# Kernel optimization log

Measured on AMD Instinct MI355X. Metric: run time of the kernel, lower is better.

Reference implementation:

```python
import jax, jax.numpy as jnp
import numpy as np

N_NODES = 100000


def _gcn_layer(h, W, b, src, dst, norm, n):
    # h: [N, Fin] -> [N, Fout]; normalized scatter-add aggregation (GCNConv)
    hw = h @ W
    msg = norm[:, None] * hw[src]
    out = jax.ops.segment_sum(msg, dst, num_segments=n)
    return out + b


def setup_inputs() -> dict:
    key = jax.random.key(0)
    k = jax.random.split(key, 10)
    N, E, P, F = N_NODES, 3200000, 500000, 128
    x = jax.random.normal(k[0], (N, F), dtype=jnp.float32)
    edge_index = jax.random.randint(k[1], (2, E), 0, N, dtype=jnp.int64)
    pred_edges = jax.random.randint(k[2], (P, 2), 0, N, dtype=jnp.int64)
    # Glorot-ish init for learned params
    W1 = jax.random.normal(k[3], (F, 16), dtype=jnp.float32) / np.sqrt(F)
    b1 = jnp.zeros((16,), dtype=jnp.float32)
    W2 = jax.random.normal(k[4], (16, 8), dtype=jnp.float32) / np.sqrt(16.0)
    b2 = jnp.zeros((8,), dtype=jnp.float32)
    Wl = jax.random.normal(k[5], (8, 1), dtype=jnp.float32) / np.sqrt(8.0)
    bl = jnp.zeros((1,), dtype=jnp.float32)
    return {"x": x, "edge_index": edge_index, "pred_edges": pred_edges,
            "W1": W1, "b1": b1, "W2": W2, "b2": b2, "Wl": Wl, "bl": bl}


def reference(x, edge_index, pred_edges, W1, b1, W2, b2, Wl, bl):
    n = x.shape[0]
    # GCN norm with self-loops: A_hat = D^{-1/2}(A+I)D^{-1/2}
    loop = jnp.arange(n, dtype=edge_index.dtype)
    src = jnp.concatenate([edge_index[0], loop])
    dst = jnp.concatenate([edge_index[1], loop])
    deg = jax.ops.segment_sum(jnp.ones_like(dst, dtype=x.dtype), dst, num_segments=n)
    dinv = jnp.where(deg > 0, jax.lax.rsqrt(deg), 0.0)
    norm = dinv[src] * dinv[dst]

    h = _gcn_layer(x, W1, b1, src, dst, norm, n)   # [N, 16]
    h = _gcn_layer(h, W2, b2, src, dst, norm, n)   # [N, 8]
    z = jax.nn.sigmoid(h @ Wl + bl)                # [N, 1]
    m = z[pred_edges]                              # [P, 2, 1]
    pred = m[:, 0, 0] * m[:, 1, 0]                 # [P]
    return pred
```

## Files before the change

kernel.cpp:

```cpp
#include <hip/hip_runtime.h>
#include <hip/hip_fp16.h>
#include <math.h>

#define BSHIFT 8
#define BUCK   256
#define TILE   8192
#define CAP    12288

typedef _Float16 f16x2 __attribute__((ext_vector_type(2)));
typedef _Float16 f16x4 __attribute__((ext_vector_type(4)));
typedef _Float16 f16x8 __attribute__((ext_vector_type(8)));
typedef float    f32x4 __attribute__((ext_vector_type(4)));


__global__ __launch_bounds__(256) void k_curinit(int* __restrict__ bcursor, int nbuk) {
    int b = blockIdx.x * 256 + threadIdx.x;
    if (b < nbuk) bcursor[b] = b * CAP;
}

__global__ __launch_bounds__(1024) void k_binscatter(const int* __restrict__ src,
                                                     const int* __restrict__ dst,
                                                     int* __restrict__ bcursor,
                                                     int* __restrict__ binned, int E, int nbuk) {
    __shared__ int            payload[TILE];
    __shared__ unsigned short bid16[TILE];
    __shared__ int cnt[512];
    __shared__ int lstart[512];
    __shared__ int gbase[512];
    __shared__ int wsum[8];
    int t = threadIdx.x;
    int tile0 = blockIdx.x * TILE;
    int tileE = min(TILE, E - tile0);
    if (t < 512) cnt[t] = 0;
    __syncthreads();
    int d[8], s[8];
    int base = t * 8;
    if (base + 8 <= tileE) {
        const int4* d4 = (const int4*)(dst + tile0 + base);
        const int4* s4 = (const int4*)(src + tile0 + base);
        int4 da = d4[0], db = d4[1];
        int4 sa = s4[0], sb = s4[1];
        d[0] = da.x; d[1] = da.y; d[2] = da.z; d[3] = da.w;
        d[4] = db.x; d[5] = db.y; d[6] = db.z; d[7] = db.w;
        s[0] = sa.x; s[1] = sa.y; s[2] = sa.z; s[3] = sa.w;
        s[4] = sb.x; s[5] = sb.y; s[6] = sb.z; s[7] = sb.w;
    } else {
#pragma unroll
        for (int q = 0; q < 8; ++q) {
            int idx = base + q;
            if (idx < tileE) { d[q] = dst[tile0 + idx]; s[q] = src[tile0 + idx]; }
            else d[q] = -1;
        }
    }
#pragma unroll
    for (int q = 0; q < 8; ++q)
        if (d[q] >= 0) atomicAdd(&cnt[d[q] >> BSHIFT], 1);
    __syncthreads();
    int c = 0, ex = 0;
    if (t < 512) {
        c = cnt[t];
        int v = c;
#pragma unroll
        for (int off = 1; off < 64; off <<= 1) {
            int u = __shfl_up(v, off, 64);
            if ((t & 63) >= off) v += u;
        }
        if ((t & 63) == 63) wsum[t >> 6] = v;
        ex = v - c;
    }
    __syncthreads();
    if (t == 0) {
        int run = 0;
#pragma unroll
        for (int w = 0; w < 8; ++w) { int u = wsum[w]; wsum[w] = run; run += u; }
    }
    __syncthreads();
    if (t < 512) {
        ex += wsum[t >> 6];
        gbase[t] = c ? atomicAdd(&bcursor[t], c) : 0;
        lstart[t] = ex;
        cnt[t] = ex;
    }
    __syncthreads();
#pragma unroll
    for (int q = 0; q < 8; ++q) {
        if (d[q] >= 0) {
            int b = d[q] >> BSHIFT;
            int lp = atomicAdd(&cnt[b], 1);
            payload[lp] = ((d[q] & (BUCK - 1)) << 17) | s[q];
            bid16[lp] = (unsigned short)b;
        }
    }
    __syncthreads();
    for (int k = t; k < tileE; k += 1024) {
        int b = bid16[k];
        int ga = gbase[b] + (k - lstart[b]);
        if (ga < (b + 1) * CAP)
            binned[ga] = payload[k];
    }
}

__global__ __launch_bounds__(1024) void k_sortbucket(const int* __restrict__ bcursor,
                                                     const int* __restrict__ binned,
                                                     int* __restrict__ csr_src,
                                                     int* __restrict__ rowstart,
                                                     int* __restrict__ rowend,
                                                     float* __restrict__ dinv, int N) {
    __shared__ int cnt[BUCK];
    __shared__ int cur[BUCK];
    __shared__ int wsum[4];
    int b = blockIdx.x, t = threadIdx.x;
    if (t < BUCK) cnt[t] = 0;
    __syncthreads();
    int beg = b * CAP;
    int end = min(bcursor[b], beg + CAP);
    int v[12];
#pragma unroll
    for (int q = 0; q < 12; ++q) {
        int e = beg + q * 1024 + t;
        v[q] = (e < end) ? binned[e] : -1;
    }
#pragma unroll
    for (int q = 0; q < 12; ++q)
        if (v[q] >= 0) atomicAdd(&cnt[v[q] >> 17], 1);
    __syncthreads();
    int c = 0, ex = 0;
    if (t < BUCK) {
        c = cnt[t];
        int s = c;
#pragma unroll
        for (int off = 1; off < 64; off <<= 1) {
            int u = __shfl_up(s, off, 64);
            if ((t & 63) >= off) s += u;
        }
        if ((t & 63) == 63) wsum[t >> 6] = s;
        ex = s - c;
    }
    __syncthreads();
    if (t == 0) {
        int run = 0;
#pragma unroll
        for (int w = 0; w < 4; ++w) { int u = wsum[w]; wsum[w] = run; run += u; }
    }
    __syncthreads();
    if (t < BUCK) {
        ex += wsum[t >> 6];
        cur[t] = ex;
        int node = b * BUCK + t;
        if (node < N) {
            rowstart[node] = beg + ex;
            rowend[node]   = beg + ex + c;
            dinv[node] = rsqrtf((float)(c + 1));
        }
    }
    __syncthreads();
#pragma unroll
    for (int q = 0; q < 12; ++q) {
        if (v[q] >= 0) {
            int pos = atomicAdd(&cur[v[q] >> 17], 1);
            csr_src[beg + pos] = v[q] & 0x1FFFF;
        }
    }
}


__global__ __launch_bounds__(256) void k_gemm1(const float* __restrict__ x,
                                               const float* __restrict__ W1,
                                               const float* __restrict__ dinv,
                                               __half* __restrict__ hw1h, int N) {
    __shared__ _Float16 sX[64 * 136];
    __shared__ _Float16 sW[16 * 136];
    __shared__ float    sDi[64];
    __shared__ _Float16 sOut[64 * 16];
    int t = threadIdx.x;
    int row0 = blockIdx.x * 64;
    for (int e = t; e < 2048; e += 256) {
        int n = e & 15, k = e >> 4;
        sW[n * 136 + k] = (_Float16)W1[k * 16 + n];
    }
    const float4* x4 = (const float4*)x;
#pragma unroll
    for (int q = 0; q < 8; ++q) {
        int e = q * 256 + t;
        int r = e >> 5, c4 = e & 31;
        int gr = row0 + r;
        float4 v = (gr < N) ? x4[(size_t)gr * 32 + c4] : make_float4(0.f, 0.f, 0.f, 0.f);
        f16x4 hv = {(_Float16)v.x, (_Float16)v.y, (_Float16)v.z, (_Float16)v.w};
        *(f16x4*)&sX[r * 136 + c4 * 4] = hv;
    }
    if (t < 64) sDi[t] = (row0 + t < N) ? dinv[row0 + t] : 0.f;
    __syncthreads();
    int w = t >> 6, l = t & 63;
    int m = l & 15, quad = l >> 4;
    f32x4 acc = {0.f, 0.f, 0.f, 0.f};
#pragma unroll
    for (int kc = 0; kc < 4; ++kc) {
        f16x8 a = *(const f16x8*)&sX[(w * 16 + m) * 136 + kc * 32 + quad * 8];
        f16x8 b = *(const f16x8*)&sW[m * 136 + kc * 32 + quad * 8];
        acc = __builtin_amdgcn_mfma_f32_16x16x32_f16(a, b, acc, 0, 0, 0);
    }
#pragma unroll
    for (int r = 0; r < 4; ++r) {
        int nl = w * 16 + quad * 4 + r;
        sOut[nl * 16 + m] = (_Float16)(acc[r] * sDi[nl]);
    }
    __syncthreads();
    int nn = t >> 2, ch = t & 3;
    int gn = row0 + nn;
    if (gn < N)
        *(float2*)&hw1h[(size_t)gn * 16 + ch * 4] = *(float2*)&sOut[nn * 16 + ch * 4];
}

__global__ __launch_bounds__(256) void k_agg1c(const int* __restrict__ rowstart,
                                               const int* __restrict__ rowend,
                                               const int* __restrict__ csr_src,
                                               const f16x8* __restrict__ hw1v,
                                               const float* __restrict__ W2,
                                               const float* __restrict__ b1,
                                               __half* __restrict__ hw2h, int N) {
    __shared__ float sW[128], sb[16];
    int t = threadIdx.x;
    if (t < 128) sW[t] = W2[t];
    if (t < 16)  sb[t] = b1[t];
    __syncthreads();
    int q = t >> 2, j = t & 3;
    int i = blockIdx.x * 64 + q;
    if (i >= N) return;
    int beg = rowstart[i], end = rowend[i];
    float di = rsqrtf((float)(end - beg + 1));
    float a[16];
#pragma unroll
    for (int d = 0; d < 16; ++d) a[d] = 0.f;
    int c0 = beg;
    for (; c0 + 16 <= end; c0 += 16) {
        int s4[4];
#pragma unroll
        for (int m = 0; m < 4; ++m) s4[m] = csr_src[c0 + 4 * j + m];
        f16x8 lo[4], hi[4];
#pragma unroll
        for (int m = 0; m < 4; ++m) {
            lo[m] = hw1v[2 * (size_t)s4[m]];
            hi[m] = hw1v[2 * (size_t)s4[m] + 1];
        }
#pragma unroll
        for (int m = 0; m < 4; ++m) {
#pragma unroll
            for (int d = 0; d < 8; ++d) {
                a[d]     += (float)lo[m][d];
                a[8 + d] += (float)hi[m][d];
            }
        }
    }
    for (int c = c0 + j; c < end; c += 4) {
        int s = csr_src[c];
        f16x8 lo = hw1v[2 * (size_t)s];
        f16x8 hi = hw1v[2 * (size_t)s + 1];
#pragma unroll
        for (int d = 0; d < 8; ++d) {
            a[d]     += (float)lo[d];
            a[8 + d] += (float)hi[d];
        }
    }
    if (j == 0) {
        f16x8 lo = hw1v[2 * (size_t)i];
        f16x8 hi = hw1v[2 * (size_t)i + 1];
#pragma unroll
        for (int d = 0; d < 8; ++d) {
            a[d]     += (float)lo[d];
            a[8 + d] += (float)hi[d];
        }
    }
#pragma unroll
    for (int d = 0; d < 16; ++d) a[d] += __shfl_xor(a[d], 1, 4);
#pragma unroll
    for (int d = 0; d < 16; ++d) a[d] += __shfl_xor(a[d], 2, 4);
    float o0 = 0.f, o1 = 0.f;
#pragma unroll
    for (int k = 0; k < 16; ++k) {
        float hv = di * a[k] + sb[k];
        o0 += hv * sW[k * 8 + 2 * j];
        o1 += hv * sW[k * 8 + 2 * j + 1];
    }
    f16x2 ho = {(_Float16)(di * o0), (_Float16)(di * o1)};
    *(f16x2*)&hw2h[(size_t)i * 8 + 2 * j] = ho;
}

__global__ __launch_bounds__(256) void k_agg2c(const int* __restrict__ rowstart,
                                               const int* __restrict__ rowend,
                                               const int* __restrict__ csr_src,
                                               const f16x8* __restrict__ hw2v,
                                               const float* __restrict__ Wl,
                                               const float* __restrict__ b2,
                                               const float* __restrict__ bl,
                                               float* __restrict__ z, int N) {
    __shared__ float sW[8], sb[8], sbl;
    int t = threadIdx.x;
    if (t < 8) { sW[t] = Wl[t]; sb[t] = b2[t]; }
    if (t == 0) sbl = bl[0];
    __syncthreads();
    int q = t >> 2, j = t & 3;
    int i = blockIdx.x * 64 + q;
    if (i >= N) return;
    int beg = rowstart[i], end = rowend[i];
    float di = rsqrtf((float)(end - beg + 1));
    float a[8];
#pragma unroll
    for (int d = 0; d < 8; ++d) a[d] = 0.f;
    int c0 = beg;
    for (; c0 + 16 <= end; c0 += 16) {
        int s4[4];
#pragma unroll
        for (int m = 0; m < 4; ++m) s4[m] = csr_src[c0 + 4 * j + m];
        f16x8 gv[4];
#pragma unroll
        for (int m = 0; m < 4; ++m) gv[m] = hw2v[(size_t)s4[m]];
#pragma unroll
        for (int m = 0; m < 4; ++m)
#pragma unroll
            for (int d = 0; d < 8; ++d) a[d] += (float)gv[m][d];
    }
    for (int c = c0 + j; c < end; c += 4) {
        f16x8 gv = hw2v[(size_t)csr_src[c]];
#pragma unroll
        for (int d = 0; d < 8; ++d) a[d] += (float)gv[d];
    }
    if (j == 0) {
        f16x8 self = hw2v[(size_t)i];
#pragma unroll
        for (int d = 0; d < 8; ++d) a[d] += (float)self[d];
    }
#pragma unroll
    for (int d = 0; d < 8; ++d) a[d] += __shfl_xor(a[d], 1, 4);
#pragma unroll
    for (int d = 0; d < 8; ++d) a[d] += __shfl_xor(a[d], 2, 4);
    if (j == 0) {
        float v = 0.f;
#pragma unroll
        for (int d = 0; d < 8; ++d) {
            float h = di * a[d] + sb[d];
            v += h * sW[d];
        }
        z[i] = 1.f / (1.f + __expf(-(v + sbl)));
    }
}

__global__ __launch_bounds__(256) void k_pred(const int2* __restrict__ pe2,
                                              const float* __restrict__ z,
                                              float* __restrict__ out, int P) {
    int p = blockIdx.x * 256 + threadIdx.x;
    if (p < P) {
        int2 e = pe2[p];
        out[p] = z[e.x] * z[e.y];
    }
}


extern "C" void kernel_launch(void* const* d_in, const int* in_sizes, int n_in,
                              void* d_out, int out_size, void* d_ws, size_t ws_size,
                              hipStream_t stream) {
    const float* x  = (const float*)d_in[0];
    const int*   ei = (const int*)d_in[1];
    const int*   pe = (const int*)d_in[2];
    const float* W1 = (const float*)d_in[3];
    const float* b1 = (const float*)d_in[4];
    const float* W2 = (const float*)d_in[5];
    const float* b2 = (const float*)d_in[6];
    const float* Wl = (const float*)d_in[7];
    const float* bl = (const float*)d_in[8];
    float* out = (float*)d_out;

    const int N = in_sizes[0] / 128;
    const int E = in_sizes[1] / 2;
    const int P = in_sizes[2] / 2;
    const int NBUK = (N + BUCK - 1) >> BSHIFT;

    const int* src = ei;
    const int* dst = ei + E;

    float*  ws   = (float*)d_ws;
    float*  dinv = ws;
    __half* hw1h = (__half*)(ws + (size_t)N);
    __half* hw2h = (__half*)(ws + (size_t)9 * N);
    float*  z    = ws + (size_t)13 * N;
    int* rowstart = (int*)(ws + (size_t)14 * N);
    int* rowend   = rowstart + N;
    int* bcursor  = rowend + N;
    int* binned   = bcursor + 512;
    int* csr_src  = binned + (size_t)NBUK * CAP;

    const int B = 256;

    k_curinit<<<(NBUK + B - 1) / B, B, 0, stream>>>(bcursor, NBUK);
    k_binscatter<<<(E + TILE - 1) / TILE, 1024, 0, stream>>>(src, dst, bcursor, binned, E, NBUK);
    k_sortbucket<<<NBUK, 1024, 0, stream>>>(bcursor, binned, csr_src, rowstart, rowend, dinv, N);
    k_gemm1<<<(N + 63) / 64, B, 0, stream>>>(x, W1, dinv, hw1h, N);
    k_agg1c<<<(N + 63) / 64, B, 0, stream>>>(rowstart, rowend, csr_src,
                                             (const f16x8*)hw1h, W2, b1, hw2h, N);
    k_agg2c<<<(N + 63) / 64, B, 0, stream>>>(rowstart, rowend, csr_src,
                                             (const f16x8*)hw2h, Wl, b2, bl, z, N);
    k_pred<<<(P + B - 1) / B, B, 0, stream>>>((const int2*)pe, z, out, P);
}
```

Baseline: 210.5 us.

## Fuse bucket sort and first GEMM into one launch, move dinv scaling to aggregation

Merges the CSR bucket-sort kernel and the x@W1 MFMA GEMM into one grid, with block ranges selected by blockIdx and shared memory overlaid through a union. The GEMM no longer depends on dinv, so both can run concurrently and one launch plus its serialization is removed. In exchange, the per-source dinv scaling moves into the first aggregation kernel, which adds an extra gathered load and multiply per edge. Each GEMM block now uses 1024 threads, covering four 64-row tiles with the padding reduced to 132.

```diff
diff --git a/kernel.cpp b/kernel.cpp
--- a/kernel.cpp
+++ b/kernel.cpp
@@ -100,120 +100,129 @@
     }
 }
 
-__global__ __launch_bounds__(1024) void k_sortbucket(const int* __restrict__ bcursor,
-                                                     const int* __restrict__ binned,
-                                                     int* __restrict__ csr_src,
-                                                     int* __restrict__ rowstart,
-                                                     int* __restrict__ rowend,
-                                                     float* __restrict__ dinv, int N) {
-    __shared__ int cnt[BUCK];
-    __shared__ int cur[BUCK];
-    __shared__ int wsum[4];
-    int b = blockIdx.x, t = threadIdx.x;
-    if (t < BUCK) cnt[t] = 0;
-    __syncthreads();
-    int beg = b * CAP;
-    int end = min(bcursor[b], beg + CAP);
-    int v[12];
-#pragma unroll
-    for (int q = 0; q < 12; ++q) {
-        int e = beg + q * 1024 + t;
-        v[q] = (e < end) ? binned[e] : -1;
-    }
-#pragma unroll
-    for (int q = 0; q < 12; ++q)
-        if (v[q] >= 0) atomicAdd(&cnt[v[q] >> 17], 1);
-    __syncthreads();
-    int c = 0, ex = 0;
-    if (t < BUCK) {
-        c = cnt[t];
-        int s = c;
-#pragma unroll
-        for (int off = 1; off < 64; off <<= 1) {
-            int u = __shfl_up(s, off, 64);
-            if ((t & 63) >= off) s += u;
-        }
-        if ((t & 63) == 63) wsum[t >> 6] = s;
-        ex = s - c;
-    }
-    __syncthreads();
-    if (t == 0) {
-        int run = 0;
-#pragma unroll
-        for (int w = 0; w < 4; ++w) { int u = wsum[w]; wsum[w] = run; run += u; }
-    }
-    __syncthreads();
-    if (t < BUCK) {
-        ex += wsum[t >> 6];
-        cur[t] = ex;
-        int node = b * BUCK + t;
-        if (node < N) {
-            rowstart[node] = beg + ex;
-            rowend[node]   = beg + ex + c;
-            dinv[node] = rsqrtf((float)(c + 1));
-        }
-    }
-    __syncthreads();
-#pragma unroll
-    for (int q = 0; q < 12; ++q) {
-        if (v[q] >= 0) {
-            int pos = atomicAdd(&cur[v[q] >> 17], 1);
-            csr_src[beg + pos] = v[q] & 0x1FFFF;
-        }
-    }
-}
-
-
-__global__ __launch_bounds__(256) void k_gemm1(const float* __restrict__ x,
-                                               const float* __restrict__ W1,
-                                               const float* __restrict__ dinv,
-                                               __half* __restrict__ hw1h, int N) {
-    __shared__ _Float16 sX[64 * 136];
-    __shared__ _Float16 sW[16 * 136];
-    __shared__ float    sDi[64];
-    __shared__ _Float16 sOut[64 * 16];
+
+union FatSmem {
+    struct { int cnt[BUCK]; int cur[BUCK]; int wsum[4]; } s;
+    struct { _Float16 sX[4][64 * 132];
+             _Float16 sW[16 * 132];
+             _Float16 sOut[4][64 * 16]; } g;
+};
+
+__global__ __launch_bounds__(1024) void k_fat(const int* __restrict__ bcursor,
+                                              const int* __restrict__ binned,
+                                              int* __restrict__ csr_src,
+                                              int* __restrict__ rowstart,
+                                              int* __restrict__ rowend,
+                                              float* __restrict__ dinv,
+                                              const float* __restrict__ x,
+                                              const float* __restrict__ W1,
+                                              __half* __restrict__ hw1h,
+                                              int N, int nbuk) {
+    __shared__ FatSmem sm;
     int t = threadIdx.x;
-    int row0 = blockIdx.x * 64;
-    for (int e = t; e < 2048; e += 256) {
-        int n = e & 15, k = e >> 4;
-        sW[n * 136 + k] = (_Float16)W1[k * 16 + n];
-    }
-    const float4* x4 = (const float4*)x;
-#pragma unroll
-    for (int q = 0; q < 8; ++q) {
-        int e = q * 256 + t;
-        int r = e >> 5, c4 = e & 31;
-        int gr = row0 + r;
-        float4 v = (gr < N) ? x4[(size_t)gr * 32 + c4] : make_float4(0.f, 0.f, 0.f, 0.f);
-        f16x4 hv = {(_Float16)v.x, (_Float16)v.y, (_Float16)v.z, (_Float16)v.w};
-        *(f16x4*)&sX[r * 136 + c4 * 4] = hv;
-    }
-    if (t < 64) sDi[t] = (row0 + t < N) ? dinv[row0 + t] : 0.f;
-    __syncthreads();
-    int w = t >> 6, l = t & 63;
-    int m = l & 15, quad = l >> 4;
-    f32x4 acc = {0.f, 0.f, 0.f, 0.f};
-#pragma unroll
-    for (int kc = 0; kc < 4; ++kc) {
-        f16x8 a = *(const f16x8*)&sX[(w * 16 + m) * 136 + kc * 32 + quad * 8];
-        f16x8 b = *(const f16x8*)&sW[m * 136 + kc * 32 + quad * 8];
-        acc = __builtin_amdgcn_mfma_f32_16x16x32_f16(a, b, acc, 0, 0, 0);
-    }
-#pragma unroll
-    for (int r = 0; r < 4; ++r) {
-        int nl = w * 16 + quad * 4 + r;
-        sOut[nl * 16 + m] = (_Float16)(acc[r] * sDi[nl]);
-    }
-    __syncthreads();
-    int nn = t >> 2, ch = t & 3;
-    int gn = row0 + nn;
-    if (gn < N)
-        *(float2*)&hw1h[(size_t)gn * 16 + ch * 4] = *(float2*)&sOut[nn * 16 + ch * 4];
-}
+    int bx = blockIdx.x;
+    if (bx < nbuk) {
+        int b = bx;
+        if (t < BUCK) sm.s.cnt[t] = 0;
+        __syncthreads();
+        int beg = b * CAP;
+        int end = min(bcursor[b], beg + CAP);
+        int v[12];
+#pragma unroll
+        for (int q = 0; q < 12; ++q) {
+            int e = beg + q * 1024 + t;
+            v[q] = (e < end) ? binned[e] : -1;
+        }
+#pragma unroll
+        for (int q = 0; q < 12; ++q)
+            if (v[q] >= 0) atomicAdd(&sm.s.cnt[v[q] >> 17], 1);
+        __syncthreads();
+        int c = 0, ex = 0;
+        if (t < BUCK) {
+            c = sm.s.cnt[t];
+            int sv = c;
+#pragma unroll
+            for (int off = 1; off < 64; off <<= 1) {
+                int u = __shfl_up(sv, off, 64);
+                if ((t & 63) >= off) sv += u;
+            }
+            if ((t & 63) == 63) sm.s.wsum[t >> 6] = sv;
+            ex = sv - c;
+        }
+        __syncthreads();
+        if (t == 0) {
+            int run = 0;
+#pragma unroll
+            for (int w = 0; w < 4; ++w) { int u = sm.s.wsum[w]; sm.s.wsum[w] = run; run += u; }
+        }
+        __syncthreads();
+        if (t < BUCK) {
+            ex += sm.s.wsum[t >> 6];
+            sm.s.cur[t] = ex;
+            int node = b * BUCK + t;
+            if (node < N) {
+                rowstart[node] = beg + ex;
+                rowend[node]   = beg + ex + c;
+                dinv[node] = rsqrtf((float)(c + 1));
+            }
+        }
+        __syncthreads();
+#pragma unroll
+        for (int q = 0; q < 12; ++q) {
+            if (v[q] >= 0) {
+                int pos = atomicAdd(&sm.s.cur[v[q] >> 17], 1);
+                csr_src[beg + pos] = v[q] & 0x1FFFF;
+            }
+        }
+    } else {
+        int gb = bx - nbuk;
+        int sub = t >> 8, tt = t & 255;
+        _Float16* sX   = sm.g.sX[sub];
+        _Float16* sW   = sm.g.sW;
+        _Float16* sOut = sm.g.sOut[sub];
+        int row0 = gb * 256 + sub * 64;
+        for (int e = t; e < 2048; e += 1024) {
+            int n = e & 15, k = e >> 4;
+            sW[n * 132 + k] = (_Float16)W1[k * 16 + n];
+        }
+        const float4* x4 = (const float4*)x;
+#pragma unroll
+        for (int q = 0; q < 8; ++q) {
+            int e = q * 256 + tt;
+            int r = e >> 5, c4 = e & 31;
+            int gr = row0 + r;
+            float4 v = (gr < N) ? x4[(size_t)gr * 32 + c4] : make_float4(0.f, 0.f, 0.f, 0.f);
+            f16x4 hv = {(_Float16)v.x, (_Float16)v.y, (_Float16)v.z, (_Float16)v.w};
+            *(f16x4*)&sX[r * 132 + c4 * 4] = hv;
+        }
+        __syncthreads();
+        int w = tt >> 6, l = tt & 63;
+        int m = l & 15, quad = l >> 4;
+        f32x4 acc = {0.f, 0.f, 0.f, 0.f};
+#pragma unroll
+        for (int kc = 0; kc < 4; ++kc) {
+            f16x8 a = *(const f16x8*)&sX[(w * 16 + m) * 132 + kc * 32 + quad * 8];
+            f16x8 bb = *(const f16x8*)&sW[m * 132 + kc * 32 + quad * 8];
+            acc = __builtin_amdgcn_mfma_f32_16x16x32_f16(a, bb, acc, 0, 0, 0);
+        }
+#pragma unroll
+        for (int r = 0; r < 4; ++r) {
+            int nl = w * 16 + quad * 4 + r;
+            sOut[nl * 16 + m] = (_Float16)acc[r];
+        }
+        __syncthreads();
+        int nn = tt >> 2, ch = tt & 3;
+        int gn = row0 + nn;
+        if (gn < N)
+            *(float2*)&hw1h[(size_t)gn * 16 + ch * 4] = *(float2*)&sOut[nn * 16 + ch * 4];
+    }
+}
+
 
 __global__ __launch_bounds__(256) void k_agg1c(const int* __restrict__ rowstart,
                                                const int* __restrict__ rowend,
                                                const int* __restrict__ csr_src,
+                                               const float* __restrict__ dinv_g,
                                                const f16x8* __restrict__ hw1v,
                                                const float* __restrict__ W2,
                                                const float* __restrict__ b1,
@@ -236,9 +245,11 @@
         int s4[4];
 #pragma unroll
         for (int m = 0; m < 4; ++m) s4[m] = csr_src[c0 + 4 * j + m];
+        float ds[4];
         f16x8 lo[4], hi[4];
 #pragma unroll
         for (int m = 0; m < 4; ++m) {
+            ds[m] = dinv_g[s4[m]];
             lo[m] = hw1v[2 * (size_t)s4[m]];
             hi[m] = hw1v[2 * (size_t)s4[m] + 1];
         }
@@ -246,19 +257,20 @@
         for (int m = 0; m < 4; ++m) {
 #pragma unroll
             for (int d = 0; d < 8; ++d) {
-                a[d]     += (float)lo[m][d];
-                a[8 + d] += (float)hi[m][d];
+                a[d]     += ds[m] * (float)lo[m][d];
+                a[8 + d] += ds[m] * (float)hi[m][d];
             }
         }
     }
     for (int c = c0 + j; c < end; c += 4) {
         int s = csr_src[c];
+        float dsv = dinv_g[s];
         f16x8 lo = hw1v[2 * (size_t)s];
         f16x8 hi = hw1v[2 * (size_t)s + 1];
 #pragma unroll
         for (int d = 0; d < 8; ++d) {
-            a[d]     += (float)lo[d];
-            a[8 + d] += (float)hi[d];
+            a[d]     += dsv * (float)lo[d];
+            a[8 + d] += dsv * (float)hi[d];
         }
     }
     if (j == 0) {
@@ -266,8 +278,8 @@
         f16x8 hi = hw1v[2 * (size_t)i + 1];
 #pragma unroll
         for (int d = 0; d < 8; ++d) {
-            a[d]     += (float)lo[d];
-            a[8 + d] += (float)hi[d];
+            a[d]     += di * (float)lo[d];
+            a[8 + d] += di * (float)hi[d];
         }
     }
 #pragma unroll
@@ -389,12 +401,13 @@
     int* csr_src  = binned + (size_t)NBUK * CAP;
 
     const int B = 256;
+    const int GGEMM = (N + 255) / 256;
 
     k_curinit<<<(NBUK + B - 1) / B, B, 0, stream>>>(bcursor, NBUK);
     k_binscatter<<<(E + TILE - 1) / TILE, 1024, 0, stream>>>(src, dst, bcursor, binned, E, NBUK);
-    k_sortbucket<<<NBUK, 1024, 0, stream>>>(bcursor, binned, csr_src, rowstart, rowend, dinv, N);
-    k_gemm1<<<(N + 63) / 64, B, 0, stream>>>(x, W1, dinv, hw1h, N);
-    k_agg1c<<<(N + 63) / 64, B, 0, stream>>>(rowstart, rowend, csr_src,
+    k_fat<<<NBUK + GGEMM, 1024, 0, stream>>>(bcursor, binned, csr_src, rowstart, rowend, dinv,
+                                             x, W1, hw1h, N, NBUK);
+    k_agg1c<<<(N + 63) / 64, B, 0, stream>>>(rowstart, rowend, csr_src, dinv,
                                              (const f16x8*)hw1h, W2, b1, hw2h, N);
     k_agg2c<<<(N + 63) / 64, B, 0, stream>>>(rowstart, rowend, csr_src,
                                              (const f16x8*)hw2h, Wl, b2, bl, z, N);
```

Result: slower. 223.3 us (+6.1%).

## Pad CSR rows to multiples of sixteen and vectorize index loads with prefetch

Applied to the files above, without the earlier changes.

Row segments in the CSR build are padded to sixteen-entry boundaries and the padding is filled with the node's own index, keeping every row 16-aligned and its tail gathers in bounds. Both aggregation kernels then read neighbor indices as int4 vectors, prefetch the next chunk's indices while the current gathers are in flight, and replace the scalar tail loop with one masked four-wide chunk. This aims to cut index-load instructions and tail divergence. The cost is extra bucket capacity use (overflow is now clamped against CAP) and some wasted gathers for padded slots.

```diff
diff --git a/kernel.cpp b/kernel.cpp
--- a/kernel.cpp
+++ b/kernel.cpp
@@ -124,17 +124,18 @@
     for (int q = 0; q < 12; ++q)
         if (v[q] >= 0) atomicAdd(&cnt[v[q] >> 17], 1);
     __syncthreads();
-    int c = 0, ex = 0;
+    int c = 0, p = 0, ex = 0;
     if (t < BUCK) {
         c = cnt[t];
-        int s = c;
+        p = (c + 15) & ~15;
+        int s = p;
 #pragma unroll
         for (int off = 1; off < 64; off <<= 1) {
             int u = __shfl_up(s, off, 64);
             if ((t & 63) >= off) s += u;
         }
         if ((t & 63) == 63) wsum[t >> 6] = s;
-        ex = s - c;
+        ex = s - p;
     }
     __syncthreads();
     if (t == 0) {
@@ -151,6 +152,8 @@
             rowstart[node] = beg + ex;
             rowend[node]   = beg + ex + c;
             dinv[node] = rsqrtf((float)(c + 1));
+            for (int pp = c; pp < p && ex + pp < CAP; ++pp)
+                csr_src[beg + ex + pp] = node;
         }
     }
     __syncthreads();
@@ -158,7 +161,7 @@
     for (int q = 0; q < 12; ++q) {
         if (v[q] >= 0) {
             int pos = atomicAdd(&cur[v[q] >> 17], 1);
-            csr_src[beg + pos] = v[q] & 0x1FFFF;
+            if (pos < CAP) csr_src[beg + pos] = v[q] & 0x1FFFF;
         }
     }
 }
@@ -227,21 +230,26 @@
     int i = blockIdx.x * 64 + q;
     if (i >= N) return;
     int beg = rowstart[i], end = rowend[i];
-    float di = rsqrtf((float)(end - beg + 1));
+    int deg = end - beg;
+    float di = rsqrtf((float)(deg + 1));
     float a[16];
 #pragma unroll
     for (int d = 0; d < 16; ++d) a[d] = 0.f;
-    int c0 = beg;
-    for (; c0 + 16 <= end; c0 += 16) {
-        int s4[4];
-#pragma unroll
-        for (int m = 0; m < 4; ++m) s4[m] = csr_src[c0 + 4 * j + m];
+    int nfull = deg >> 4;
+    int base0 = beg + 4 * j;
+    int4 s4;
+    if (nfull > 0) s4 = *(const int4*)&csr_src[base0];
+    for (int ch = 0; ch < nfull; ++ch) {
+        int sv[4] = {s4.x, s4.y, s4.z, s4.w};
         f16x8 lo[4], hi[4];
 #pragma unroll
         for (int m = 0; m < 4; ++m) {
-            lo[m] = hw1v[2 * (size_t)s4[m]];
-            hi[m] = hw1v[2 * (size_t)s4[m] + 1];
-        }
+            lo[m] = hw1v[2 * (size_t)sv[m]];
+            hi[m] = hw1v[2 * (size_t)sv[m] + 1];
+        }
+        int4 sn;
+        if (ch + 1 < nfull)
+            sn = *(const int4*)&csr_src[base0 + (ch + 1) * 16];
 #pragma unroll
         for (int m = 0; m < 4; ++m) {
 #pragma unroll
@@ -250,15 +258,26 @@
                 a[8 + d] += (float)hi[m][d];
             }
         }
-    }
-    for (int c = c0 + j; c < end; c += 4) {
-        int s = csr_src[c];
-        f16x8 lo = hw1v[2 * (size_t)s];
-        f16x8 hi = hw1v[2 * (size_t)s + 1];
-#pragma unroll
-        for (int d = 0; d < 8; ++d) {
-            a[d]     += (float)lo[d];
-            a[8 + d] += (float)hi[d];
+        if (ch + 1 < nfull) s4 = sn;
+    }
+    if (deg & 15) {
+        int cb = base0 + nfull * 16;
+        int4 st = *(const int4*)&csr_src[cb];
+        int   sr[4] = {st.x, st.y, st.z, st.w};
+        f16x8 lo[4], hi[4];
+#pragma unroll
+        for (int m = 0; m < 4; ++m) {
+            lo[m] = hw1v[2 * (size_t)sr[m]];
+            hi[m] = hw1v[2 * (size_t)sr[m] + 1];
+        }
+#pragma unroll
+        for (int m = 0; m < 4; ++m) {
+            float wr = (cb + m < end) ? 1.f : 0.f;
+#pragma unroll
+            for (int d = 0; d < 8; ++d) {
+                a[d]     += wr * (float)lo[m][d];
+                a[8 + d] += wr * (float)hi[m][d];
+            }
         }
     }
     if (j == 0) {
@@ -302,27 +321,42 @@
     int i = blockIdx.x * 64 + q;
     if (i >= N) return;
     int beg = rowstart[i], end = rowend[i];
-    float di = rsqrtf((float)(end - beg + 1));
+    int deg = end - beg;
+    float di = rsqrtf((float)(deg + 1));
     float a[8];
 #pragma unroll
     for (int d = 0; d < 8; ++d) a[d] = 0.f;
-    int c0 = beg;
-    for (; c0 + 16 <= end; c0 += 16) {
-        int s4[4];
-#pragma unroll
-        for (int m = 0; m < 4; ++m) s4[m] = csr_src[c0 + 4 * j + m];
+    int nfull = deg >> 4;
+    int base0 = beg + 4 * j;
+    int4 s4;
+    if (nfull > 0) s4 = *(const int4*)&csr_src[base0];
+    for (int ch = 0; ch < nfull; ++ch) {
+        int sv[4] = {s4.x, s4.y, s4.z, s4.w};
         f16x8 gv[4];
 #pragma unroll
-        for (int m = 0; m < 4; ++m) gv[m] = hw2v[(size_t)s4[m]];
+        for (int m = 0; m < 4; ++m) gv[m] = hw2v[(size_t)sv[m]];
+        int4 sn;
+        if (ch + 1 < nfull)
+            sn = *(const int4*)&csr_src[base0 + (ch + 1) * 16];
 #pragma unroll
         for (int m = 0; m < 4; ++m)
 #pragma unroll
             for (int d = 0; d < 8; ++d) a[d] += (float)gv[m][d];
-    }
-    for (int c = c0 + j; c < end; c += 4) {
-        f16x8 gv = hw2v[(size_t)csr_src[c]];
-#pragma unroll
-        for (int d = 0; d < 8; ++d) a[d] += (float)gv[d];
+        if (ch + 1 < nfull) s4 = sn;
+    }
+    if (deg & 15) {
+        int cb = base0 + nfull * 16;
+        int4 st = *(const int4*)&csr_src[cb];
+        int sr[4] = {st.x, st.y, st.z, st.w};
+        f16x8 gv[4];
+#pragma unroll
+        for (int m = 0; m < 4; ++m) gv[m] = hw2v[(size_t)sr[m]];
+#pragma unroll
+        for (int m = 0; m < 4; ++m) {
+            float wr = (cb + m < end) ? 1.f : 0.f;
+#pragma unroll
+            for (int d = 0; d < 8; ++d) a[d] += wr * (float)gv[m][d];
+        }
     }
     if (j == 0) {
         f16x8 self = hw2v[(size_t)i];
```

After: 210.0 us. Within noise of the previous version (-0.2%).

## Pad CSR rows to 16-aligned and split feature halves across lanes in aggregation

Applied to the files above, without the earlier changes.

The bucket sort now pads each node's CSR segment to a multiple of 16 entries, filling the padding with the node's own index, so aggregation kernels can read neighbour indices with aligned int4 loads. In both aggregation kernels, lanes are split into pairs: one pair strides over edges and each lane of a pair gathers one half of the feature vector. Each lane then holds fewer accumulators, and the halves are exchanged by shuffle before the small dense projection. Padding raises bucket occupancy and could overflow CAP, which is guarded. The tail chunk masks padded entries with a weight of zero.

```diff
diff --git a/kernel.cpp b/kernel.cpp
--- a/kernel.cpp
+++ b/kernel.cpp
@@ -124,17 +124,18 @@
     for (int q = 0; q < 12; ++q)
         if (v[q] >= 0) atomicAdd(&cnt[v[q] >> 17], 1);
     __syncthreads();
-    int c = 0, ex = 0;
+    int c = 0, p = 0, ex = 0;
     if (t < BUCK) {
         c = cnt[t];
-        int s = c;
+        p = (c + 15) & ~15;
+        int s = p;
 #pragma unroll
         for (int off = 1; off < 64; off <<= 1) {
             int u = __shfl_up(s, off, 64);
             if ((t & 63) >= off) s += u;
         }
         if ((t & 63) == 63) wsum[t >> 6] = s;
-        ex = s - c;
+        ex = s - p;
     }
     __syncthreads();
     if (t == 0) {
@@ -151,6 +152,8 @@
             rowstart[node] = beg + ex;
             rowend[node]   = beg + ex + c;
             dinv[node] = rsqrtf((float)(c + 1));
+            for (int pp = c; pp < p && ex + pp < CAP; ++pp)
+                csr_src[beg + ex + pp] = node;
         }
     }
     __syncthreads();
@@ -158,7 +161,7 @@
     for (int q = 0; q < 12; ++q) {
         if (v[q] >= 0) {
             int pos = atomicAdd(&cur[v[q] >> 17], 1);
-            csr_src[beg + pos] = v[q] & 0x1FFFF;
+            if (pos < CAP) csr_src[beg + pos] = v[q] & 0x1FFFF;
         }
     }
 }
@@ -224,62 +227,82 @@
     if (t < 16)  sb[t] = b1[t];
     __syncthreads();
     int q = t >> 2, j = t & 3;
+    int j2 = j & 1, j4 = j >> 1;
     int i = blockIdx.x * 64 + q;
     if (i >= N) return;
     int beg = rowstart[i], end = rowend[i];
-    float di = rsqrtf((float)(end - beg + 1));
-    float a[16];
-#pragma unroll
-    for (int d = 0; d < 16; ++d) a[d] = 0.f;
-    int c0 = beg;
-    for (; c0 + 16 <= end; c0 += 16) {
-        int s4[4];
-#pragma unroll
-        for (int m = 0; m < 4; ++m) s4[m] = csr_src[c0 + 4 * j + m];
-        f16x8 lo[4], hi[4];
+    int deg = end - beg;
+    float di = rsqrtf((float)(deg + 1));
+    float a[8];
+#pragma unroll
+    for (int d = 0; d < 8; ++d) a[d] = 0.f;
+    int nfull = deg >> 3;
+    int lbase = beg + 4 * j4;
+    int ch = 0;
+    for (; ch + 2 <= nfull; ch += 2) {
+        int4 ia = *(const int4*)&csr_src[lbase + 8 * ch];
+        int4 ib = *(const int4*)&csr_src[lbase + 8 * (ch + 1)];
+        int sa[4] = {ia.x, ia.y, ia.z, ia.w};
+        int sc[4] = {ib.x, ib.y, ib.z, ib.w};
+        f16x8 ga[4], gb[4];
+#pragma unroll
+        for (int m = 0; m < 4; ++m) ga[m] = hw1v[2 * (size_t)sa[m] + j2];
+#pragma unroll
+        for (int m = 0; m < 4; ++m) gb[m] = hw1v[2 * (size_t)sc[m] + j2];
+#pragma unroll
+        for (int m = 0; m < 4; ++m)
+#pragma unroll
+            for (int d = 0; d < 8; ++d)
+                a[d] += (float)ga[m][d] + (float)gb[m][d];
+    }
+    if (ch < nfull) {
+        int4 ia = *(const int4*)&csr_src[lbase + 8 * ch];
+        int sa[4] = {ia.x, ia.y, ia.z, ia.w};
+        f16x8 ga[4];
+#pragma unroll
+        for (int m = 0; m < 4; ++m) ga[m] = hw1v[2 * (size_t)sa[m] + j2];
+#pragma unroll
+        for (int m = 0; m < 4; ++m)
+#pragma unroll
+            for (int d = 0; d < 8; ++d) a[d] += (float)ga[m][d];
+    }
+    if (deg & 7) {
+        int cb = lbase + 8 * nfull;
+        int4 ia = *(const int4*)&csr_src[cb];
+        int sa[4] = {ia.x, ia.y, ia.z, ia.w};
+        f16x8 ga[4];
+#pragma unroll
+        for (int m = 0; m < 4; ++m) ga[m] = hw1v[2 * (size_t)sa[m] + j2];
 #pragma unroll
         for (int m = 0; m < 4; ++m) {
-            lo[m] = hw1v[2 * (size_t)s4[m]];
-            hi[m] = hw1v[2 * (size_t)s4[m] + 1];
-        }
-#pragma unroll
-        for (int m = 0; m < 4; ++m) {
-#pragma unroll
-            for (int d = 0; d < 8; ++d) {
-                a[d]     += (float)lo[m][d];
-                a[8 + d] += (float)hi[m][d];
-            }
-        }
-    }
-    for (int c = c0 + j; c < end; c += 4) {
-        int s = csr_src[c];
-        f16x8 lo = hw1v[2 * (size_t)s];
-        f16x8 hi = hw1v[2 * (size_t)s + 1];
-#pragma unroll
-        for (int d = 0; d < 8; ++d) {
-            a[d]     += (float)lo[d];
-            a[8 + d] += (float)hi[d];
-        }
-    }
-    if (j == 0) {
-        f16x8 lo = hw1v[2 * (size_t)i];
-        f16x8 hi = hw1v[2 * (size_t)i + 1];
-#pragma unroll
-        for (int d = 0; d < 8; ++d) {
-            a[d]     += (float)lo[d];
-            a[8 + d] += (float)hi[d];
-        }
-    }
-#pragma unroll
-    for (int d = 0; d < 16; ++d) a[d] += __shfl_xor(a[d], 1, 4);
-#pragma unroll
-    for (int d = 0; d < 16; ++d) a[d] += __shfl_xor(a[d], 2, 4);
+            float wr = (cb + m < end) ? 1.f : 0.f;
+#pragma unroll
+            for (int d = 0; d < 8; ++d) a[d] += wr * (float)ga[m][d];
+        }
+    }
+    if (j4 == 0) {
+        f16x8 sv = hw1v[2 * (size_t)i + j2];
+#pragma unroll
+        for (int d = 0; d < 8; ++d) a[d] += (float)sv[d];
+    }
+#pragma unroll
+    for (int d = 0; d < 8; ++d) a[d] += __shfl_xor(a[d], 2, 4);
+    float bo[8];
+#pragma unroll
+    for (int d = 0; d < 8; ++d) bo[d] = __shfl_xor(a[d], 1, 4);
+    int oo = 8 * j2, ot = 8 - oo;
     float o0 = 0.f, o1 = 0.f;
 #pragma unroll
-    for (int k = 0; k < 16; ++k) {
-        float hv = di * a[k] + sb[k];
-        o0 += hv * sW[k * 8 + 2 * j];
-        o1 += hv * sW[k * 8 + 2 * j + 1];
+    for (int d = 0; d < 8; ++d) {
+        float hv = di * a[d] + sb[oo + d];
+        o0 += hv * sW[(oo + d) * 8 + 2 * j];
+        o1 += hv * sW[(oo + d) * 8 + 2 * j + 1];
+    }
+#pragma unroll
+    for (int d = 0; d < 8; ++d) {
+        float hv = di * bo[d] + sb[ot + d];
+        o0 += hv * sW[(ot + d) * 8 + 2 * j];
+        o1 += hv * sW[(ot + d) * 8 + 2 * j + 1];
     }
     f16x2 ho = {(_Float16)(di * o0), (_Float16)(di * o1)};
     *(f16x2*)&hw2h[(size_t)i * 8 + 2 * j] = ho;
@@ -288,7 +311,7 @@
 __global__ __launch_bounds__(256) void k_agg2c(const int* __restrict__ rowstart,
                                                const int* __restrict__ rowend,
                                                const int* __restrict__ csr_src,
-                                               const f16x8* __restrict__ hw2v,
+                                               const f16x4* __restrict__ hw2q,
                                                const float* __restrict__ Wl,
                                                const float* __restrict__ b2,
                                                const float* __restrict__ bl,
@@ -299,49 +322,83 @@
     if (t == 0) sbl = bl[0];
     __syncthreads();
     int q = t >> 2, j = t & 3;
+    int j2 = j & 1, j4 = j >> 1;
     int i = blockIdx.x * 64 + q;
     if (i >= N) return;
     int beg = rowstart[i], end = rowend[i];
-    float di = rsqrtf((float)(end - beg + 1));
-    float a[8];
-#pragma unroll
-    for (int d = 0; d < 8; ++d) a[d] = 0.f;
-    int c0 = beg;
-    for (; c0 + 16 <= end; c0 += 16) {
-        int s4[4];
-#pragma unroll
-        for (int m = 0; m < 4; ++m) s4[m] = csr_src[c0 + 4 * j + m];
-        f16x8 gv[4];
-#pragma unroll
-        for (int m = 0; m < 4; ++m) gv[m] = hw2v[(size_t)s4[m]];
+    int deg = end - beg;
+    float di = rsqrtf((float)(deg + 1));
+    float a[4];
+#pragma unroll
+    for (int d = 0; d < 4; ++d) a[d] = 0.f;
+    int nfull = deg >> 3;
+    int lbase = beg + 4 * j4;
+    int ch = 0;
+    for (; ch + 2 <= nfull; ch += 2) {
+        int4 ia = *(const int4*)&csr_src[lbase + 8 * ch];
+        int4 ib = *(const int4*)&csr_src[lbase + 8 * (ch + 1)];
+        int sa[4] = {ia.x, ia.y, ia.z, ia.w};
+        int sc[4] = {ib.x, ib.y, ib.z, ib.w};
+        f16x4 ga[4], gb[4];
+#pragma unroll
+        for (int m = 0; m < 4; ++m) ga[m] = hw2q[2 * (size_t)sa[m] + j2];
+#pragma unroll
+        for (int m = 0; m < 4; ++m) gb[m] = hw2q[2 * (size_t)sc[m] + j2];
 #pragma unroll
         for (int m = 0; m < 4; ++m)
 #pragma unroll
-            for (int d = 0; d < 8; ++d) a[d] += (float)gv[m][d];
-    }
-    for (int c = c0 + j; c < end; c += 4) {
-        f16x8 gv = hw2v[(size_t)csr_src[c]];
-#pragma unroll
-        for (int d = 0; d < 8; ++d) a[d] += (float)gv[d];
-    }
-    if (j == 0) {
-        f16x8 self = hw2v[(size_t)i];
-#pragma unroll
-        for (int d = 0; d < 8; ++d) a[d] += (float)self[d];
-    }
-#pragma unroll
-    for (int d = 0; d < 8; ++d) a[d] += __shfl_xor(a[d], 1, 4);
-#pragma unroll
-    for (int d = 0; d < 8; ++d) a[d] += __shfl_xor(a[d], 2, 4);
-    if (j == 0) {
-        float v = 0.f;
-#pragma unroll
-        for (int d = 0; d < 8; ++d) {
-            float h = di * a[d] + sb[d];
-            v += h * sW[d];
-        }
+            for (int d = 0; d < 4; ++d)
+                a[d] += (float)ga[m][d] + (float)gb[m][d];
+    }
+    if (ch < nfull) {
+        int4 ia = *(const int4*)&csr_src[lbase + 8 * ch];
+        int sa[4] = {ia.x, ia.y, ia.z, ia.w};
+        f16x4 ga[4];
+#pragma unroll
+        for (int m = 0; m < 4; ++m) ga[m] = hw2q[2 * (size_t)sa[m] + j2];
+#pragma unroll
+        for (int m = 0; m < 4; ++m)
+#pragma unroll
+            for (int d = 0; d < 4; ++d) a[d] += (float)ga[m][d];
+    }
+    if (deg & 7) {
+        int cb = lbase + 8 * nfull;
+        int4 ia = *(const int4*)&csr_src[cb];
+        int sa[4] = {ia.x, ia.y, ia.z, ia.w};
+        f16x4 ga[4];
+#pragma unroll
+        for (int m = 0; m < 4; ++m) ga[m] = hw2q[2 * (size_t)sa[m] + j2];
+#pragma unroll
+        for (int m = 0; m < 4; ++m) {
+            float wr = (cb + m < end) ? 1.f : 0.f;
+#pragma unroll
+            for (int d = 0; d < 4; ++d) a[d] += wr * (float)ga[m][d];
+        }
+    }
+    if (j4 == 0) {
+        f16x4 sv = hw2q[2 * (size_t)i + j2];
+#pragma unroll
+        for (int d = 0; d < 4; ++d) a[d] += (float)sv[d];
+    }
+#pragma unroll
+    for (int d = 0; d < 4; ++d) a[d] += __shfl_xor(a[d], 2, 4);
+    float bo[4];
+#pragma unroll
+    for (int d = 0; d < 4; ++d) bo[d] = __shfl_xor(a[d], 1, 4);
+    int oo = 4 * j2, ot = 4 - oo;
+    float v = 0.f;
+#pragma unroll
+    for (int d = 0; d < 4; ++d) {
+        float h = di * a[d] + sb[oo + d];
+        v += h * sW[oo + d];
+    }
+#pragma unroll
+    for (int d = 0; d < 4; ++d) {
+        float h = di * bo[d] + sb[ot + d];
+        v += h * sW[ot + d];
+    }
+    if (j == 0)
         z[i] = 1.f / (1.f + __expf(-(v + sbl)));
-    }
 }
 
 __global__ __launch_bounds__(256) void k_pred(const int2* __restrict__ pe2,
@@ -397,6 +454,6 @@
     k_agg1c<<<(N + 63) / 64, B, 0, stream>>>(rowstart, rowend, csr_src,
                                              (const f16x8*)hw1h, W2, b1, hw2h, N);
     k_agg2c<<<(N + 63) / 64, B, 0, stream>>>(rowstart, rowend, csr_src,
-                                             (const f16x8*)hw2h, Wl, b2, bl, z, N);
+                                             (const f16x4*)hw2h, Wl, b2, bl, z, N);
     k_pred<<<(P + B - 1) / B, B, 0, stream>>>((const int2*)pe, z, out, P);
 }
```

New measurement: 209.4 us. No clear change (-0.5%).
